# Kernel tuning notes

Hardware: AMD Instinct MI355X
Metric: run time of the kernel (lower is better)

## Reference

```python
import jax, jax.numpy as jnp
import numpy as np

N_NODES = 50000
N_EDGES = 800000
D_IN = 256
D_HID = 256
D_OUT = 256


def setup_inputs() -> dict:
    key = jax.random.key(0)
    ks = jax.random.split(key, 14)
    s = 1.0 / np.sqrt(D_IN)
    inp = {
        "x": jax.random.normal(ks[0], (N_NODES, D_IN), dtype=jnp.float32),
        "edge_index": jax.random.randint(ks[1], (2, N_EDGES), 0, N_NODES, dtype=jnp.int64),
        "edge_attr": jax.random.uniform(ks[2], (N_EDGES, 1), dtype=jnp.float32),
        # GCNConv layer weights (3 layers)
        "W1": jax.random.normal(ks[3], (D_IN, D_HID), dtype=jnp.float32) * s,
        "b1": jnp.zeros((D_HID,), dtype=jnp.float32),
        "W2": jax.random.normal(ks[4], (D_HID, D_HID), dtype=jnp.float32) * s,
        "b2": jnp.zeros((D_HID,), dtype=jnp.float32),
        "W3": jax.random.normal(ks[5], (D_HID, D_OUT), dtype=jnp.float32) * s,
        "b3": jnp.zeros((D_OUT,), dtype=jnp.float32),
        # edge MLP: Linear(1,8) -> ReLU -> Linear(8,1) -> Sigmoid
        "mw1": jax.random.normal(ks[6], (1, 8), dtype=jnp.float32),
        "mb1": jnp.zeros((8,), dtype=jnp.float32),
        "mw2": jax.random.normal(ks[7], (8, 1), dtype=jnp.float32) * (1.0 / np.sqrt(8.0)),
        "mb2": jnp.zeros((1,), dtype=jnp.float32),
    }
    return inp


def _gcn_layer(x, src, dst, ew, W, b, n):
    """PyG GCNConv: add self-loops (weight 1), symmetric normalization."""
    deg = jax.ops.segment_sum(ew, dst, num_segments=n) + 1.0  # self-loop contributes 1
    dinv = jax.lax.rsqrt(deg)                                 # [N]
    norm = dinv[src] * ew * dinv[dst]                         # [E]
    h = x @ W + b                                             # [N, d_out]
    agg = jax.ops.segment_sum(h[src] * norm[:, None], dst, num_segments=n)
    # self-loop term: dinv[i] * 1 * dinv[i] = 1/deg[i]
    return agg + h * (1.0 / deg)[:, None]


def reference(x, edge_index, edge_attr, W1, b1, W2, b2, W3, b3, mw1, mb1, mw2, mb2):
    src, dst = edge_index[0], edge_index[1]
    # edge weight MLP with sigmoid gate
    h = jax.nn.relu(edge_attr @ mw1 + mb1)
    ew = jax.nn.sigmoid(h @ mw2 + mb2)[:, 0]  # [E]

    n = x.shape[0]
    x = jax.nn.relu(_gcn_layer(x, src, dst, ew, W1, b1, n))  # dropout inactive (eval)
    x = jax.nn.relu(_gcn_layer(x, src, dst, ew, W2, b2, n))
    x = _gcn_layer(x, src, dst, ew, W3, b3, n)
    return x
```

## Files before the change

kernel.cpp:

```cpp
#include <hip/hip_runtime.h>
#include <hip/hip_bf16.h>
#include <stdint.h>

#define GCN_N 50000
#define GCN_E 800000
#define GCN_D 256

typedef __attribute__((ext_vector_type(8))) short bf16x8;
typedef __attribute__((ext_vector_type(4))) float f32x4;
typedef unsigned short ushort_t;
typedef unsigned long long u64;

__device__ __forceinline__ float bf2f(ushort_t u) {
    return __uint_as_float(((unsigned)u) << 16);
}
__device__ __forceinline__ ushort_t f2bf(float f) {
    unsigned v = __float_as_uint(f);
    v += 0x7FFFu + ((v >> 16) & 1u);
    return (ushort_t)(v >> 16);
}


__global__ void init_kernel(u64* dc, int n) {
    int i = blockIdx.x * blockDim.x + threadIdx.x;
    if (i < n) dc[i] = 0ull;
}

__global__ void edge_mlp_kernel(const float* __restrict__ attr,
                                const int* __restrict__ dst,
                                const float* __restrict__ mw1, const float* __restrict__ mb1,
                                const float* __restrict__ mw2, const float* __restrict__ mb2,
                                float* __restrict__ ew, u64* __restrict__ dc,
                                int* __restrict__ rank, int e_count) {
    int e = blockIdx.x * blockDim.x + threadIdx.x;
    if (e >= e_count) return;
    float a = attr[e];
    float s = mb2[0];
#pragma unroll
    for (int j = 0; j < 8; ++j) {
        float hj = fmaf(a, mw1[j], mb1[j]);
        hj = fmaxf(hj, 0.0f);
        s = fmaf(hj, mw2[j], s);
    }
    float w = 1.0f / (1.0f + expf(-s));
    ew[e] = w;
    u64 pack = (1ull << 40) + (u64)((double)w * 4294967296.0);
    u64 old = atomicAdd(&dc[dst[e]], pack);
    rank[e] = (int)(old >> 40);
}

__global__ void node_kernel(const u64* __restrict__ dc, float* __restrict__ dinv,
                            float* __restrict__ invdeg, int n) {
    int i = blockIdx.x * blockDim.x + threadIdx.x;
    if (i < n) {
        u64 v = dc[i];
        float wsum = (float)((double)(v & ((1ull << 40) - 1)) * (1.0 / 4294967296.0));
        float d = 1.0f + wsum;
        dinv[i] = rsqrtf(d);
        invdeg[i] = 1.0f / d;
    }
}

__global__ __launch_bounds__(1024) void scan1_kernel(const u64* __restrict__ dc,
                                                     int* __restrict__ part,
                                                     int* __restrict__ bsum, int n) {
    __shared__ int s[1024];
    int tid = threadIdx.x;
    int i = blockIdx.x * 1024 + tid;
    int v = (i < n) ? (int)(dc[i] >> 40) : 0;
    s[tid] = v;
    __syncthreads();
#pragma unroll
    for (int d = 1; d < 1024; d <<= 1) {
        int t = (tid >= d) ? s[tid - d] : 0;
        __syncthreads();
        s[tid] += t;
        __syncthreads();
    }
    if (i < n) part[i] = s[tid] - v;
    if (tid == 1023) bsum[blockIdx.x] = s[1023];
}

__global__ void scan2_kernel(int* bsum, int nb) {
    int t = threadIdx.x;
    int orig = (t < nb) ? bsum[t] : 0;
    int v = orig;
#pragma unroll
    for (int d = 1; d < 64; d <<= 1) {
        int u = __shfl_up(v, d, 64);
        if (t >= d) v += u;
    }
    if (t < nb) bsum[t] = v - orig;
}

__global__ void scan3_kernel(const int* __restrict__ part, const int* __restrict__ bsum,
                             int* __restrict__ offs, int n, int e_total) {
    int i = blockIdx.x * blockDim.x + threadIdx.x;
    if (i < n) offs[i] = part[i] + bsum[i >> 10];
    if (i == 0) offs[n] = e_total;
}

__global__ void scatter_kernel(const int* __restrict__ src, const int* __restrict__ dst,
                               const float* __restrict__ ew, const float* __restrict__ dinv,
                               const int* __restrict__ offs, const int* __restrict__ rank,
                               int2* __restrict__ csr, int e_count) {
    int e = blockIdx.x * blockDim.x + threadIdx.x;
    if (e >= e_count) return;
    int sN = src[e], dN = dst[e];
    int pos = offs[dN] + rank[e];
    float w = dinv[sN] * ew[e] * dinv[dN];
    csr[pos] = make_int2(sN, __float_as_int(w));
}


__global__ __launch_bounds__(256) void wconvert_kernel(const float* __restrict__ W,
                                                       ushort_t* __restrict__ wtf_hi,
                                                       ushort_t* __restrict__ wtf_lo) {
    __shared__ ushort_t lds_hi[32][256];
    __shared__ ushort_t lds_lo[32][256];
    const int kt = blockIdx.x;
    const int tid = threadIdx.x;
    for (int c = 0; c < 32; ++c) {
        float f = W[(kt * 32 + c) * GCN_D + tid];
        unsigned u = __float_as_uint(f);
        ushort_t hi = (ushort_t)(u >> 16);
        float r = f - __uint_as_float(u & 0xFFFF0000u);
        lds_hi[c][tid] = hi;
        lds_lo[c][tid] = f2bf(r);
    }
    __syncthreads();
#pragma unroll
    for (int q = 0; q < 4; ++q) {
        int slot = q * 256 + tid;
        int lane = slot & 63, nt = slot >> 6;
        int n = nt * 16 + (lane & 15);
        int kl = (lane >> 4) * 8;
        ushort_t h8[8], l8[8];
#pragma unroll
        for (int j = 0; j < 8; ++j) { h8[j] = lds_hi[kl + j][n]; l8[j] = lds_lo[kl + j][n]; }
        size_t o = ((size_t)(kt * 16 + nt) * 64 + lane) * 8;
#pragma unroll
        for (int j = 0; j < 8; ++j) { wtf_hi[o + j] = h8[j]; wtf_lo[o + j] = l8[j]; }
    }
}


__device__ __forceinline__ void split_f32x8(float4 f0, float4 f1, bf16x8& hi, bf16x8& lo) {
    float f[8] = {f0.x, f0.y, f0.z, f0.w, f1.x, f1.y, f1.z, f1.w};
#pragma unroll
    for (int i = 0; i < 8; ++i) {
        unsigned u = __float_as_uint(f[i]);
        hi[i] = (short)(u >> 16);
        float r = f[i] - __uint_as_float(u & 0xFFFF0000u);
        lo[i] = (short)f2bf(r);
    }
}

__global__ __launch_bounds__(256) void mfma_gemm_f32_kernel(
        const float* __restrict__ x,
        const ushort_t* __restrict__ wtf_hi,
        const ushort_t* __restrict__ wtf_lo,
        const float* __restrict__ bias,
        ushort_t* __restrict__ out_h,
        int n_rows) {
    __shared__ ushort_t smem[4 * 16 * 264];
    const int tid  = threadIdx.x;
    const int lane = tid & 63;
    const int wv   = tid >> 6;
    const int r16  = lane & 15;
    const int kg   = lane >> 4;
    const int row0 = blockIdx.x * 64 + wv * 16;

    f32x4 acc[16];
#pragma unroll
    for (int nt = 0; nt < 16; ++nt) acc[nt] = (f32x4){0.f, 0.f, 0.f, 0.f};

    const int arow = row0 + r16;
    const float* ap = (arow < n_rows) ? &x[(size_t)arow * GCN_D + kg * 8] : nullptr;
    bf16x8* sH = (bf16x8*)smem;
    bf16x8* sL = ((bf16x8*)smem) + 1024;

#pragma unroll 1
    for (int kt = 0; kt < 8; ++kt) {
        float4 f0 = make_float4(0.f, 0.f, 0.f, 0.f), f1 = f0;
        if (ap) {
            f0 = *(const float4*)(ap + kt * 32);
            f1 = *(const float4*)(ap + kt * 32 + 4);
        }
        const bf16x8* gh = (const bf16x8*)wtf_hi + (size_t)kt * 1024;
        const bf16x8* gl = (const bf16x8*)wtf_lo + (size_t)kt * 1024;
        bf16x8 t0 = gh[tid], t1 = gh[256 + tid], t2 = gh[512 + tid], t3 = gh[768 + tid];
        bf16x8 u0 = gl[tid], u1 = gl[256 + tid], u2 = gl[512 + tid], u3 = gl[768 + tid];
        sH[tid] = t0; sH[256 + tid] = t1; sH[512 + tid] = t2; sH[768 + tid] = t3;
        sL[tid] = u0; sL[256 + tid] = u1; sL[512 + tid] = u2; sL[768 + tid] = u3;
        bf16x8 a_hi, a_lo;
        split_f32x8(f0, f1, a_hi, a_lo);
        __syncthreads();
#pragma unroll
        for (int nt = 0; nt < 16; ++nt) {
            bf16x8 bh = sH[nt * 64 + lane];
            bf16x8 bl = sL[nt * 64 + lane];
            acc[nt] = __builtin_amdgcn_mfma_f32_16x16x32_bf16(a_hi, bh, acc[nt], 0, 0, 0);
            acc[nt] = __builtin_amdgcn_mfma_f32_16x16x32_bf16(a_lo, bh, acc[nt], 0, 0, 0);
            acc[nt] = __builtin_amdgcn_mfma_f32_16x16x32_bf16(a_hi, bl, acc[nt], 0, 0, 0);
        }
        __syncthreads();
    }

    ushort_t* my = smem + wv * (16 * 264);
#pragma unroll
    for (int nt = 0; nt < 16; ++nt) {
        float bv = bias[nt * 16 + r16];
#pragma unroll
        for (int r = 0; r < 4; ++r)
            my[(kg * 4 + r) * 264 + nt * 16 + r16] = f2bf(acc[nt][r] + bv);
    }
#pragma unroll 4
    for (int r = 0; r < 16; ++r) {
        int row = row0 + r;
        if (row < n_rows) {
            ushort4 v = *(ushort4*)&my[r * 264 + lane * 4];
            *(ushort4*)&out_h[(size_t)row * GCN_D + lane * 4] = v;
        }
    }
}


__global__ __launch_bounds__(256) void mfma_gemm_bf16_kernel(
        const ushort_t* __restrict__ a_in,
        const ushort_t* __restrict__ wtf_hi,
        const float* __restrict__ bias,
        ushort_t* __restrict__ out_h,
        int n_rows) {
    __shared__ ushort_t smem[4 * 16 * 264];
    const int tid  = threadIdx.x;
    const int lane = tid & 63;
    const int wv   = tid >> 6;
    const int r16  = lane & 15;
    const int kg   = lane >> 4;
    const int row0 = blockIdx.x * 64 + wv * 16;

    f32x4 acc[16];
#pragma unroll
    for (int nt = 0; nt < 16; ++nt) acc[nt] = (f32x4){0.f, 0.f, 0.f, 0.f};

    const int arow = row0 + r16;
    const ushort_t* ap = (arow < n_rows) ? &a_in[(size_t)arow * GCN_D + kg * 8] : nullptr;
    bf16x8* sH = (bf16x8*)smem;

#pragma unroll 1
    for (int kt = 0; kt < 8; ++kt) {
        bf16x8 a = (bf16x8){0, 0, 0, 0, 0, 0, 0, 0};
        if (ap) a = *(const bf16x8*)(ap + kt * 32);
        const bf16x8* gh = (const bf16x8*)wtf_hi + (size_t)kt * 1024;
        bf16x8 t0 = gh[tid], t1 = gh[256 + tid], t2 = gh[512 + tid], t3 = gh[768 + tid];
        sH[tid] = t0; sH[256 + tid] = t1; sH[512 + tid] = t2; sH[768 + tid] = t3;
        __syncthreads();
#pragma unroll
        for (int nt = 0; nt < 16; ++nt) {
            bf16x8 bh = sH[nt * 64 + lane];
            acc[nt] = __builtin_amdgcn_mfma_f32_16x16x32_bf16(a, bh, acc[nt], 0, 0, 0);
        }
        __syncthreads();
    }

    ushort_t* my = smem + wv * (16 * 264);
#pragma unroll
    for (int nt = 0; nt < 16; ++nt) {
        float bv = bias[nt * 16 + r16];
#pragma unroll
        for (int r = 0; r < 4; ++r)
            my[(kg * 4 + r) * 264 + nt * 16 + r16] = f2bf(acc[nt][r] + bv);
    }
#pragma unroll 4
    for (int r = 0; r < 16; ++r) {
        int row = row0 + r;
        if (row < n_rows) {
            ushort4 v = *(ushort4*)&my[r * 264 + lane * 4];
            *(ushort4*)&out_h[(size_t)row * GCN_D + lane * 4] = v;
        }
    }
}


template <int OUT_BF16>
__global__ __launch_bounds__(256) void spmm_kernel(const ushort_t* __restrict__ h,
                                                   const int* __restrict__ offs,
                                                   const int2* __restrict__ csr,
                                                   const float* __restrict__ invdeg,
                                                   void* __restrict__ outp, int n) {
    int wid = (blockIdx.x * blockDim.x + threadIdx.x) >> 6;
    int lane = threadIdx.x & 63;
    if (wid >= n) return;
    const ushort4* h4 = (const ushort4*)h;
    ushort4 sv = h4[(size_t)wid * 64 + lane];
    float sw = invdeg[wid];
    float4 acc;
    acc.x = bf2f(sv.x) * sw; acc.y = bf2f(sv.y) * sw;
    acc.z = bf2f(sv.z) * sw; acc.w = bf2f(sv.w) * sw;
    int e0 = offs[wid], e1 = offs[wid + 1];
    int k = e0;
    for (; k + 16 <= e1; k += 16) {
        int2 ee[16]; ushort4 vv[16];
#pragma unroll
        for (int u = 0; u < 16; ++u) ee[u] = csr[k + u];
#pragma unroll
        for (int u = 0; u < 16; ++u) vv[u] = h4[(size_t)ee[u].x * 64 + lane];
#pragma unroll
        for (int u = 0; u < 16; ++u) {
            float w = __int_as_float(ee[u].y);
            acc.x = fmaf(w, bf2f(vv[u].x), acc.x);
            acc.y = fmaf(w, bf2f(vv[u].y), acc.y);
            acc.z = fmaf(w, bf2f(vv[u].z), acc.z);
            acc.w = fmaf(w, bf2f(vv[u].w), acc.w);
        }
    }
    if (k + 8 <= e1) {
        int2 ee[8]; ushort4 vv[8];
#pragma unroll
        for (int u = 0; u < 8; ++u) ee[u] = csr[k + u];
#pragma unroll
        for (int u = 0; u < 8; ++u) vv[u] = h4[(size_t)ee[u].x * 64 + lane];
#pragma unroll
        for (int u = 0; u < 8; ++u) {
            float w = __int_as_float(ee[u].y);
            acc.x = fmaf(w, bf2f(vv[u].x), acc.x);
            acc.y = fmaf(w, bf2f(vv[u].y), acc.y);
            acc.z = fmaf(w, bf2f(vv[u].z), acc.z);
            acc.w = fmaf(w, bf2f(vv[u].w), acc.w);
        }
        k += 8;
    }
    for (; k < e1; ++k) {
        int2 e = csr[k];
        float w = __int_as_float(e.y);
        ushort4 hv = h4[(size_t)e.x * 64 + lane];
        acc.x = fmaf(w, bf2f(hv.x), acc.x);
        acc.y = fmaf(w, bf2f(hv.y), acc.y);
        acc.z = fmaf(w, bf2f(hv.z), acc.z);
        acc.w = fmaf(w, bf2f(hv.w), acc.w);
    }
    if (OUT_BF16) {
        ushort4 o;
        o.x = f2bf(fmaxf(acc.x, 0.f));
        o.y = f2bf(fmaxf(acc.y, 0.f));
        o.z = f2bf(fmaxf(acc.z, 0.f));
        o.w = f2bf(fmaxf(acc.w, 0.f));
        ((ushort4*)outp)[(size_t)wid * 64 + lane] = o;
    } else {
        ((float4*)outp)[(size_t)wid * 64 + lane] = acc;
    }
}


extern "C" void kernel_launch(void* const* d_in, const int* in_sizes, int n_in,
                              void* d_out, int out_size, void* d_ws, size_t ws_size,
                              hipStream_t stream) {
    const float* x    = (const float*)d_in[0];
    const int*   ei   = (const int*)d_in[1];
    const float* attr = (const float*)d_in[2];
    const float* W1 = (const float*)d_in[3];  const float* b1 = (const float*)d_in[4];
    const float* W2 = (const float*)d_in[5];  const float* b2 = (const float*)d_in[6];
    const float* W3 = (const float*)d_in[7];  const float* b3 = (const float*)d_in[8];
    const float* mw1 = (const float*)d_in[9]; const float* mb1 = (const float*)d_in[10];
    const float* mw2 = (const float*)d_in[11];const float* mb2 = (const float*)d_in[12];
    float* out = (float*)d_out;

    const int N = GCN_N, E = GCN_E;
    const int* srcI = ei;
    const int* dstI = ei + E;

    char* ws = (char*)d_ws;
    float* ew     = (float*)ws;                      ws += (size_t)E * 4;
    int*   rank   = (int*)ws;                        ws += (size_t)E * 4;
    u64*   dc     = (u64*)(((uintptr_t)ws + 255) & ~(uintptr_t)255); ws = (char*)(dc + N);
    float* dinv   = (float*)ws;                      ws += (size_t)N * 4;
    float* invdeg = (float*)ws;                      ws += (size_t)N * 4;
    int*   offs   = (int*)ws;                        ws += (size_t)(N + 1) * 4;
    int*   bsum   = (int*)ws;                        ws += 64 * 4;
    int*   part   = (int*)ws;                        ws += (size_t)N * 4;
    int2*  csr    = (int2*)(((uintptr_t)ws + 255) & ~(uintptr_t)255); ws = (char*)(csr + E);
    ushort_t* h   = (ushort_t*)(((uintptr_t)ws + 255) & ~(uintptr_t)255);
    ws = (char*)(h + (size_t)N * GCN_D);
    ushort_t* act = (ushort_t*)(((uintptr_t)ws + 255) & ~(uintptr_t)255);
    ws = (char*)(act + (size_t)N * GCN_D);
    ushort_t* wtf = (ushort_t*)(((uintptr_t)ws + 255) & ~(uintptr_t)255);
    ushort_t* wtf_hi1 = wtf;
    ushort_t* wtf_lo1 = wtf + 65536;
    ushort_t* wtf_hi2 = wtf + 2 * 65536;
    ushort_t* wtf_lo2 = wtf + 3 * 65536;
    ushort_t* wtf_hi3 = wtf + 4 * 65536;
    ushort_t* wtf_lo3 = wtf + 5 * 65536;

    init_kernel<<<(N + 255) / 256, 256, 0, stream>>>(dc, N);
    edge_mlp_kernel<<<(E + 255) / 256, 256, 0, stream>>>(attr, dstI, mw1, mb1, mw2, mb2,
                                                         ew, dc, rank, E);
    node_kernel<<<(N + 255) / 256, 256, 0, stream>>>(dc, dinv, invdeg, N);
    int nb = (N + 1023) / 1024;
    scan1_kernel<<<nb, 1024, 0, stream>>>(dc, part, bsum, N);
    scan2_kernel<<<1, 64, 0, stream>>>(bsum, nb);
    scan3_kernel<<<(N + 255) / 256, 256, 0, stream>>>(part, bsum, offs, N, E);
    scatter_kernel<<<(E + 255) / 256, 256, 0, stream>>>(srcI, dstI, ew, dinv, offs, rank,
                                                        csr, E);
    wconvert_kernel<<<8, 256, 0, stream>>>(W1, wtf_hi1, wtf_lo1);
    wconvert_kernel<<<8, 256, 0, stream>>>(W2, wtf_hi2, wtf_lo2);
    wconvert_kernel<<<8, 256, 0, stream>>>(W3, wtf_hi3, wtf_lo3);

    const int gemm_grid = (N + 63) / 64;
    const int spmm_grid = (N * 64 + 255) / 256;

    mfma_gemm_f32_kernel<<<gemm_grid, 256, 0, stream>>>(x, wtf_hi1, wtf_lo1, b1, h, N);
    spmm_kernel<1><<<spmm_grid, 256, 0, stream>>>(h, offs, csr, invdeg, act, N);
    mfma_gemm_bf16_kernel<<<gemm_grid, 256, 0, stream>>>(act, wtf_hi2, b2, h, N);
    spmm_kernel<1><<<spmm_grid, 256, 0, stream>>>(h, offs, csr, invdeg, act, N);
    mfma_gemm_bf16_kernel<<<gemm_grid, 256, 0, stream>>>(act, wtf_hi3, b3, h, N);
    spmm_kernel<0><<<spmm_grid, 256, 0, stream>>>(h, offs, csr, invdeg, out, N);
}
```

Measured before the change: 356.3 us.

## Merge small preprocessing kernels, batch weight conversion, restructure GEMM k-loop

Replaces the init kernel with hipMemsetAsync and folds the node degree computation into the first scan kernel. The three weight-conversion launches become one 24-block launch, which cuts launch count and serial gaps between tiny kernels. The bf16 GEMM now stages two k-tiles per LDS barrier, halving the synchronisations but doubling the LDS staging per step. The SpMM drops its 16-wide unrolled gather and keeps only the 8-wide loop, which lowers register pressure but gives less memory-level parallelism per wave.

```diff
diff --git a/kernel.cpp b/kernel.cpp
--- a/kernel.cpp
+++ b/kernel.cpp
@@ -20,11 +20,6 @@
     return (ushort_t)(v >> 16);
 }
 
-
-__global__ void init_kernel(u64* dc, int n) {
-    int i = blockIdx.x * blockDim.x + threadIdx.x;
-    if (i < n) dc[i] = 0ull;
-}
 
 __global__ void edge_mlp_kernel(const float* __restrict__ attr,
                                 const int* __restrict__ dst,
@@ -49,26 +44,23 @@
     rank[e] = (int)(old >> 40);
 }
 
-__global__ void node_kernel(const u64* __restrict__ dc, float* __restrict__ dinv,
-                            float* __restrict__ invdeg, int n) {
-    int i = blockIdx.x * blockDim.x + threadIdx.x;
+__global__ __launch_bounds__(1024) void scan1_kernel(const u64* __restrict__ dc,
+                                                     int* __restrict__ part,
+                                                     int* __restrict__ bsum,
+                                                     float* __restrict__ dinv,
+                                                     float* __restrict__ invdeg, int n) {
+    __shared__ int s[1024];
+    int tid = threadIdx.x;
+    int i = blockIdx.x * 1024 + tid;
+    u64 dv = (i < n) ? dc[i] : 0ull;
+    int v = (int)(dv >> 40);
+    s[tid] = v;
     if (i < n) {
-        u64 v = dc[i];
-        float wsum = (float)((double)(v & ((1ull << 40) - 1)) * (1.0 / 4294967296.0));
+        float wsum = (float)((double)(dv & ((1ull << 40) - 1)) * (1.0 / 4294967296.0));
         float d = 1.0f + wsum;
         dinv[i] = rsqrtf(d);
         invdeg[i] = 1.0f / d;
     }
-}
-
-__global__ __launch_bounds__(1024) void scan1_kernel(const u64* __restrict__ dc,
-                                                     int* __restrict__ part,
-                                                     int* __restrict__ bsum, int n) {
-    __shared__ int s[1024];
-    int tid = threadIdx.x;
-    int i = blockIdx.x * 1024 + tid;
-    int v = (i < n) ? (int)(dc[i] >> 40) : 0;
-    s[tid] = v;
     __syncthreads();
 #pragma unroll
     for (int d = 1; d < 1024; d <<= 1) {
@@ -113,12 +105,17 @@
 }
 
 
-__global__ __launch_bounds__(256) void wconvert_kernel(const float* __restrict__ W,
-                                                       ushort_t* __restrict__ wtf_hi,
-                                                       ushort_t* __restrict__ wtf_lo) {
+__global__ __launch_bounds__(256) void wconvert_kernel(
+        const float* __restrict__ W1, const float* __restrict__ W2,
+        const float* __restrict__ W3,
+        ushort_t* __restrict__ wtf) {
     __shared__ ushort_t lds_hi[32][256];
     __shared__ ushort_t lds_lo[32][256];
-    const int kt = blockIdx.x;
+    const int layer = blockIdx.x >> 3;
+    const int kt = blockIdx.x & 7;
+    const float* W = (layer == 0) ? W1 : (layer == 1) ? W2 : W3;
+    ushort_t* wtf_hi = wtf + (size_t)layer * 2 * 65536;
+    ushort_t* wtf_lo = wtf_hi + 65536;
     const int tid = threadIdx.x;
     for (int c = 0; c < 32; ++c) {
         float f = W[(kt * 32 + c) * GCN_D + tid];
@@ -249,17 +246,25 @@
     bf16x8* sH = (bf16x8*)smem;
 
 #pragma unroll 1
-    for (int kt = 0; kt < 8; ++kt) {
-        bf16x8 a = (bf16x8){0, 0, 0, 0, 0, 0, 0, 0};
-        if (ap) a = *(const bf16x8*)(ap + kt * 32);
-        const bf16x8* gh = (const bf16x8*)wtf_hi + (size_t)kt * 1024;
-        bf16x8 t0 = gh[tid], t1 = gh[256 + tid], t2 = gh[512 + tid], t3 = gh[768 + tid];
-        sH[tid] = t0; sH[256 + tid] = t1; sH[512 + tid] = t2; sH[768 + tid] = t3;
+    for (int kp = 0; kp < 4; ++kp) {
+        const bf16x8* gh = (const bf16x8*)wtf_hi + (size_t)kp * 2048;
+        bf16x8 t[8];
+#pragma unroll
+        for (int j = 0; j < 8; ++j) t[j] = gh[j * 256 + tid];
+        bf16x8 a0 = (bf16x8){0,0,0,0,0,0,0,0}, a1 = a0;
+        if (ap) {
+            a0 = *(const bf16x8*)(ap + (kp * 2) * 32);
+            a1 = *(const bf16x8*)(ap + (kp * 2 + 1) * 32);
+        }
+#pragma unroll
+        for (int j = 0; j < 8; ++j) sH[j * 256 + tid] = t[j];
         __syncthreads();
 #pragma unroll
         for (int nt = 0; nt < 16; ++nt) {
-            bf16x8 bh = sH[nt * 64 + lane];
-            acc[nt] = __builtin_amdgcn_mfma_f32_16x16x32_bf16(a, bh, acc[nt], 0, 0, 0);
+            bf16x8 bh0 = sH[nt * 64 + lane];
+            bf16x8 bh1 = sH[1024 + nt * 64 + lane];
+            acc[nt] = __builtin_amdgcn_mfma_f32_16x16x32_bf16(a0, bh0, acc[nt], 0, 0, 0);
+            acc[nt] = __builtin_amdgcn_mfma_f32_16x16x32_bf16(a1, bh1, acc[nt], 0, 0, 0);
         }
         __syncthreads();
     }
@@ -300,22 +305,7 @@
     acc.z = bf2f(sv.z) * sw; acc.w = bf2f(sv.w) * sw;
     int e0 = offs[wid], e1 = offs[wid + 1];
     int k = e0;
-    for (; k + 16 <= e1; k += 16) {
-        int2 ee[16]; ushort4 vv[16];
-#pragma unroll
-        for (int u = 0; u < 16; ++u) ee[u] = csr[k + u];
-#pragma unroll
-        for (int u = 0; u < 16; ++u) vv[u] = h4[(size_t)ee[u].x * 64 + lane];
-#pragma unroll
-        for (int u = 0; u < 16; ++u) {
-            float w = __int_as_float(ee[u].y);
-            acc.x = fmaf(w, bf2f(vv[u].x), acc.x);
-            acc.y = fmaf(w, bf2f(vv[u].y), acc.y);
-            acc.z = fmaf(w, bf2f(vv[u].z), acc.z);
-            acc.w = fmaf(w, bf2f(vv[u].w), acc.w);
-        }
-    }
-    if (k + 8 <= e1) {
+    for (; k + 8 <= e1; k += 8) {
         int2 ee[8]; ushort4 vv[8];
 #pragma unroll
         for (int u = 0; u < 8; ++u) ee[u] = csr[k + u];
@@ -329,7 +319,6 @@
             acc.z = fmaf(w, bf2f(vv[u].z), acc.z);
             acc.w = fmaf(w, bf2f(vv[u].w), acc.w);
         }
-        k += 8;
     }
     for (; k < e1; ++k) {
         int2 e = csr[k];
@@ -388,23 +377,18 @@
     ushort_t* wtf_hi1 = wtf;
     ushort_t* wtf_lo1 = wtf + 65536;
     ushort_t* wtf_hi2 = wtf + 2 * 65536;
-    ushort_t* wtf_lo2 = wtf + 3 * 65536;
     ushort_t* wtf_hi3 = wtf + 4 * 65536;
-    ushort_t* wtf_lo3 = wtf + 5 * 65536;
-
-    init_kernel<<<(N + 255) / 256, 256, 0, stream>>>(dc, N);
+
+    hipMemsetAsync(dc, 0, (size_t)N * sizeof(u64), stream);
     edge_mlp_kernel<<<(E + 255) / 256, 256, 0, stream>>>(attr, dstI, mw1, mb1, mw2, mb2,
                                                          ew, dc, rank, E);
-    node_kernel<<<(N + 255) / 256, 256, 0, stream>>>(dc, dinv, invdeg, N);
     int nb = (N + 1023) / 1024;
-    scan1_kernel<<<nb, 1024, 0, stream>>>(dc, part, bsum, N);
+    scan1_kernel<<<nb, 1024, 0, stream>>>(dc, part, bsum, dinv, invdeg, N);
     scan2_kernel<<<1, 64, 0, stream>>>(bsum, nb);
     scan3_kernel<<<(N + 255) / 256, 256, 0, stream>>>(part, bsum, offs, N, E);
     scatter_kernel<<<(E + 255) / 256, 256, 0, stream>>>(srcI, dstI, ew, dinv, offs, rank,
                                                         csr, E);
-    wconvert_kernel<<<8, 256, 0, stream>>>(W1, wtf_hi1, wtf_lo1);
-    wconvert_kernel<<<8, 256, 0, stream>>>(W2, wtf_hi2, wtf_lo2);
-    wconvert_kernel<<<8, 256, 0, stream>>>(W3, wtf_hi3, wtf_lo3);
+    wconvert_kernel<<<24, 256, 0, stream>>>(W1, W2, W3, wtf);
 
     const int gemm_grid = (N + 63) / 64;
     const int spmm_grid = (N * 64 + 255) / 256;
```

After: 335.2 us. 5.9% less time.
